# Kernel tuning notes

Measured on AMD Instinct MI355X. Metric: run time of the kernel, lower is better.

The kernel has to match this reference:

```python
import jax, jax.numpy as jnp
import numpy as np

B, T, DIM, H = 2, 2048, 512, 8
EPS = 1e-6


def setup_inputs() -> dict:
    key = jax.random.key(0)
    ks = jax.random.split(key, 6)
    scale = 0.05  # keep activations in a sane range for softmax/elu
    return {
        "x": jax.random.normal(ks[0], (B, T, DIM), dtype=jnp.float32),
        "Wq": jax.random.normal(ks[1], (DIM, DIM), dtype=jnp.float32) * scale,
        "Wk": jax.random.normal(ks[2], (DIM, DIM), dtype=jnp.float32) * scale,
        "Wv": jax.random.normal(ks[3], (DIM, DIM), dtype=jnp.float32) * scale,
        "Wo": jax.random.normal(ks[4], (DIM, DIM), dtype=jnp.float32) * scale,
        "bo": jax.random.normal(ks[5], (DIM,), dtype=jnp.float32) * scale,
    }


def reference(x, Wq, Wk, Wv, Wo, bo):
    b, t, dim = x.shape
    h = H
    d = dim // h
    # projections (nn.Linear: x @ W.T)
    q = x @ Wq.T
    k = x @ Wk.T
    v = x @ Wv.T
    mh = lambda z: z.reshape(b, t, h, d).transpose(0, 2, 1, 3)  # [b,h,t,d]
    q, k, v = mh(q), mh(k), mh(v)
    # causal linear attention with buckets = n (bucket size 1, no shift)
    q = jax.nn.softmax(q, axis=-1)
    k = jax.nn.elu(k) + 1.0  # psi
    k_cumsum = jnp.cumsum(k, axis=2)                       # [b,h,t,d]
    context = jnp.einsum('bhnd,bhne->bhnde', k, v)         # per-position outer products
    context = jnp.cumsum(context, axis=2)                  # causal prefix sum, [b,h,t,d,d]
    context = context / (k_cumsum[..., None] + EPS)        # safe_div
    attn = jnp.einsum('bhnd,bhnde->bhne', q, context)      # [b,h,t,d]
    out = attn.transpose(0, 2, 1, 3).reshape(b, t, dim)
    return out @ Wo.T + bo
```

## Files before the change

### kernel.cpp

```cpp
#include <hip/hip_runtime.h>

#define T_SEQ 2048
#define DIMM 512
#define NH 8
#define HD 64
#define BB 2
#define CHUNK 64
#define NCHUNK 32
#define EPSV 1e-6f
#define LDST 72

typedef __attribute__((ext_vector_type(8))) short bf16x8;
typedef __attribute__((ext_vector_type(4))) short s16x4;
typedef __attribute__((ext_vector_type(4))) float f32x4;

static __device__ inline short f2bf(float f) {
    union { float f; unsigned u; } v; v.f = f;
    unsigned r = v.u + 0x7FFFu + ((v.u >> 16) & 1u);
    return (short)(r >> 16);
}
static __device__ inline float bf2f(short s) {
    union { unsigned u; float f; } v; v.u = ((unsigned)(unsigned short)s) << 16;
    return v.f;
}

__global__ __launch_bounds__(256) void proj_mfma_kernel(
    const float* __restrict__ x, const float* __restrict__ Wq,
    const float* __restrict__ Wk, const float* __restrict__ Wv,
    short* __restrict__ Qs, short* __restrict__ Kbf,
    short* __restrict__ Ktb, short* __restrict__ Vt)
{
    __shared__ short As[128 * LDST];
    __shared__ short Bs[128 * LDST];
    const int which = blockIdx.y >> 2;
    const float* __restrict__ W = (which == 0) ? Wq : ((which == 1) ? Wk : Wv);
    const int m0 = blockIdx.x * 128;
    const int n0 = (blockIdx.y & 3) * 128;
    const int tid = threadIdx.x;
    const int lane = tid & 63, wid = tid >> 6;
    const int wr = wid >> 1, wc = wid & 1;
    const int fr = lane & 15, fg = lane >> 4;
    const int head0 = (blockIdx.y & 3) * 2 + wc;
    f32x4 acc[4][4] = {};
    for (int k0 = 0; k0 < DIMM; k0 += 64) {
        #pragma unroll
        for (int it = 0; it < 8; it++) {
            const int qi = it * 256 + tid;
            const int r = qi >> 4, k4 = (qi & 15) << 2;
            const float4 va = *(const float4*)(x + (size_t)(m0 + r) * DIMM + k0 + k4);
            *(s16x4*)&As[r * LDST + k4] = (s16x4){f2bf(va.x), f2bf(va.y), f2bf(va.z), f2bf(va.w)};
            const float4 vb = *(const float4*)(W + (size_t)(n0 + r) * DIMM + k0 + k4);
            *(s16x4*)&Bs[r * LDST + k4] = (s16x4){f2bf(vb.x), f2bf(vb.y), f2bf(vb.z), f2bf(vb.w)};
        }
        __syncthreads();
        #pragma unroll
        for (int ks = 0; ks < 2; ks++) {
            bf16x8 af[4], bfr[4];
            #pragma unroll
            for (int i = 0; i < 4; i++)
                af[i] = *(const bf16x8*)&As[(wr * 64 + i * 16 + fr) * LDST + ks * 32 + fg * 8];
            #pragma unroll
            for (int j = 0; j < 4; j++)
                bfr[j] = *(const bf16x8*)&Bs[(wc * 64 + j * 16 + fr) * LDST + ks * 32 + fg * 8];
            #pragma unroll
            for (int i = 0; i < 4; i++)
                #pragma unroll
                for (int j = 0; j < 4; j++)
                    acc[i][j] = __builtin_amdgcn_mfma_f32_16x16x32_bf16(af[i], bfr[j], acc[i][j], 0, 0, 0);
        }
        __syncthreads();
    }
    if (which == 0) {
        #pragma unroll
        for (int i = 0; i < 4; i++) {
            #pragma unroll
            for (int reg = 0; reg < 4; reg++) {
                float v[4];
                #pragma unroll
                for (int j = 0; j < 4; j++) v[j] = acc[i][j][reg];
                float mx = fmaxf(fmaxf(v[0], v[1]), fmaxf(v[2], v[3]));
                #pragma unroll
                for (int off = 1; off <= 8; off <<= 1) mx = fmaxf(mx, __shfl_xor(mx, off, 64));
                float e[4], s = 0.f;
                #pragma unroll
                for (int j = 0; j < 4; j++) { e[j] = __expf(v[j] - mx); s += e[j]; }
                #pragma unroll
                for (int off = 1; off <= 8; off <<= 1) s += __shfl_xor(s, off, 64);
                const float inv = 1.f / s;
                const int m = m0 + wr * 64 + i * 16 + fg * 4 + reg;
                const int b = m >> 11, t = m & (T_SEQ - 1);
                short* qp = Qs + (((size_t)(b * NH + head0)) * T_SEQ + t) * HD;
                #pragma unroll
                for (int j = 0; j < 4; j++) qp[j * 16 + fr] = f2bf(e[j] * inv);
            }
        }
    } else if (which == 1) {
        #pragma unroll
        for (int i = 0; i < 4; i++) {
            const int m3 = m0 + wr * 64 + i * 16 + fg * 4;
            const int b = m3 >> 11, t0 = m3 & (T_SEQ - 1);
            #pragma unroll
            for (int j = 0; j < 4; j++) {
                const int d = j * 16 + fr;
                short kv[4];
                #pragma unroll
                for (int reg = 0; reg < 4; reg++) {
                    float val = acc[i][j][reg];
                    val = (val > 0.f) ? (val + 1.f) : __expf(val);
                    kv[reg] = f2bf(val);
                }
                short* kp = Kbf + (((size_t)(b * NH + head0)) * T_SEQ + t0) * HD + d;
                kp[0] = kv[0]; kp[HD] = kv[1]; kp[2 * HD] = kv[2]; kp[3 * HD] = kv[3];
                *(s16x4*)(Ktb + (((size_t)(b * NH + head0)) * HD + d) * T_SEQ + t0) =
                    (s16x4){kv[0], kv[1], kv[2], kv[3]};
            }
        }
    } else {
        #pragma unroll
        for (int i = 0; i < 4; i++) {
            const int m3 = m0 + wr * 64 + i * 16 + fg * 4;
            const int b = m3 >> 11, t0 = m3 & (T_SEQ - 1);
            #pragma unroll
            for (int j = 0; j < 4; j++) {
                const int e = j * 16 + fr;
                *(s16x4*)(Vt + (((size_t)(b * NH + head0)) * HD + e) * T_SEQ + t0) =
                    (s16x4){f2bf(acc[i][j][0]), f2bf(acc[i][j][1]),
                            f2bf(acc[i][j][2]), f2bf(acc[i][j][3])};
            }
        }
    }
}

__global__ __launch_bounds__(256) void chunk_sum_kernel(
    const short* __restrict__ Ktb, const short* __restrict__ Vt,
    float* __restrict__ Schunk, float* __restrict__ kchunk)
{
    __shared__ short VtL[64 * LDST];
    __shared__ short KtL[64 * LDST];
    __shared__ float ksp[4][64];
    const int bh = blockIdx.x >> 5, c = blockIdx.x & 31;
    const int tid = threadIdx.x;
    const int lane = tid & 63, w = tid >> 6;
    const int fr = lane & 15, fg = lane >> 4;
    #pragma unroll
    for (int it = 0; it < 2; it++) {
        const int qi = it * 256 + tid;
        const int r = qi >> 3, c8 = (qi & 7) * 8;
        *(bf16x8*)&VtL[r * LDST + c8] =
            *(const bf16x8*)(Vt + ((size_t)(bh * HD) + r) * T_SEQ + c * CHUNK + c8);
        *(bf16x8*)&KtL[r * LDST + c8] =
            *(const bf16x8*)(Ktb + ((size_t)(bh * HD) + r) * T_SEQ + c * CHUNK + c8);
    }
    __syncthreads();
    f32x4 acc[4] = {};
    #pragma unroll
    for (int ks = 0; ks < 2; ks++) {
        const bf16x8 av = *(const bf16x8*)&VtL[(w * 16 + fr) * LDST + ks * 32 + fg * 8];
        #pragma unroll
        for (int j = 0; j < 4; j++) {
            const bf16x8 bk = *(const bf16x8*)&KtL[(j * 16 + fr) * LDST + ks * 32 + fg * 8];
            acc[j] = __builtin_amdgcn_mfma_f32_16x16x32_bf16(av, bk, acc[j], 0, 0, 0);
        }
    }
    float* Sout = Schunk + ((size_t)bh * NCHUNK + c) * 4096;
    #pragma unroll
    for (int j = 0; j < 4; j++)
        #pragma unroll
        for (int reg = 0; reg < 4; reg++)
            Sout[(w * 16 + fg * 4 + reg) * 64 + j * 16 + fr] = acc[j][reg];
    float ps = 0.f;
    #pragma unroll
    for (int t = 0; t < 16; t++) ps += bf2f(KtL[lane * LDST + w * 16 + t]);
    ksp[w][lane] = ps;
    __syncthreads();
    if (tid < 64)
        kchunk[((size_t)bh * NCHUNK + c) * 64 + tid] =
            ksp[0][tid] + ksp[1][tid] + ksp[2][tid] + ksp[3][tid];
}

__global__ __launch_bounds__(256) void scan_kernel(float* __restrict__ Schunk,
                                                   float* __restrict__ kchunk)
{
    const int gid = blockIdx.x * 256 + threadIdx.x;
    if (blockIdx.x < 256) {
        const int bh = gid >> 12, i = gid & 4095;
        float run = 0.f;
        float* p = Schunk + (size_t)bh * NCHUNK * 4096 + i;
        for (int c = 0; c < NCHUNK; c++) { const float tv = p[c * 4096]; p[c * 4096] = run; run += tv; }
    } else {
        const int idx = gid - 65536;
        const int bh = idx >> 6, d = idx & 63;
        float run = 0.f;
        float* p = kchunk + (size_t)bh * NCHUNK * 64 + d;
        for (int c = 0; c < NCHUNK; c++) { const float tv = p[c * 64]; p[c * 64] = run; run += tv; }
    }
}

__global__ __launch_bounds__(256) void intra_kernel(
    const short* __restrict__ Qs, const short* __restrict__ Kbf,
    const short* __restrict__ Vt, const float* __restrict__ Schunk,
    const float* __restrict__ kchunk, short* __restrict__ attnb)
{
    __shared__ short B1[64 * LDST];
    __shared__ short B2[64 * LDST];
    __shared__ short KL[64 * LDST];
    __shared__ short VtL[64 * LDST];
    __shared__ short QnL[64 * LDST];
    __shared__ float gsum[4][64];
    __shared__ float kpre[64];
    const int bh = blockIdx.x >> 5, c = blockIdx.x & 31;
    const int tid = threadIdx.x;
    const int lane = tid & 63, w = tid >> 6;
    const int fr = lane & 15, fg = lane >> 4;
    const size_t tdbase = ((size_t)bh * T_SEQ + c * CHUNK) * HD;
    #pragma unroll
    for (int it = 0; it < 2; it++) {
        const int qi = it * 256 + tid;
        const int r = qi >> 3, c8 = (qi & 7) * 8;
        *(bf16x8*)&B1[r * LDST + c8]  = *(const bf16x8*)(Qs + tdbase + r * HD + c8);
        *(bf16x8*)&KL[r * LDST + c8]  = *(const bf16x8*)(Kbf + tdbase + r * HD + c8);
        *(bf16x8*)&VtL[r * LDST + c8] =
            *(const bf16x8*)(Vt + ((size_t)(bh * HD) + r) * T_SEQ + c * CHUNK + c8);
    }
    {
        const float* Sp = Schunk + ((size_t)bh * NCHUNK + c) * 4096;
        #pragma unroll
        for (int it = 0; it < 4; it++) {
            const int qi = it * 256 + tid;
            const int r = qi >> 4, c4 = (qi & 15) * 4;
            const float4 v = *(const float4*)(Sp + r * 64 + c4);
            *(s16x4*)&B2[r * LDST + c4] = (s16x4){f2bf(v.x), f2bf(v.y), f2bf(v.z), f2bf(v.w)};
        }
    }
    if (tid < 64) kpre[tid] = kchunk[((size_t)bh * NCHUNK + c) * 64 + tid];
    __syncthreads();
    {
        float s = 0.f;
        #pragma unroll
        for (int t = 0; t < 16; t++) s += bf2f(KL[(w * 16 + t) * LDST + lane]);
        gsum[w][lane] = s;
    }
    __syncthreads();
    {
        float run = kpre[lane];
        for (int gg = 0; gg < w; gg++) run += gsum[gg][lane];
        #pragma unroll
        for (int t0 = 0; t0 < 16; t0++) {
            const int t = w * 16 + t0;
            run += bf2f(KL[t * LDST + lane]);
            const float qv = bf2f(B1[t * LDST + lane]);
            QnL[t * LDST + lane] = f2bf(qv / (run + EPSV));
        }
    }
    __syncthreads();
    {
        f32x4 a1[4] = {};
        #pragma unroll
        for (int ks = 0; ks < 2; ks++) {
            const bf16x8 aq = *(const bf16x8*)&QnL[(w * 16 + fr) * LDST + ks * 32 + fg * 8];
            #pragma unroll
            for (int j = 0; j < 4; j++) {
                const bf16x8 bk = *(const bf16x8*)&KL[(j * 16 + fr) * LDST + ks * 32 + fg * 8];
                a1[j] = __builtin_amdgcn_mfma_f32_16x16x32_bf16(aq, bk, a1[j], 0, 0, 0);
            }
        }
        const int trow = w * 16 + fg * 4;
        #pragma unroll
        for (int j = 0; j < 4; j++)
            #pragma unroll
            for (int reg = 0; reg < 4; reg++) {
                const int t = trow + reg, s = j * 16 + fr;
                B1[t * LDST + s] = (s <= t) ? f2bf(a1[j][reg]) : (short)0;
            }
    }
    __syncthreads();
    {
        f32x4 a2[4] = {};
        #pragma unroll
        for (int ks = 0; ks < 2; ks++) {
            const bf16x8 aq = *(const bf16x8*)&QnL[(w * 16 + fr) * LDST + ks * 32 + fg * 8];
            const bf16x8 aa = *(const bf16x8*)&B1[(w * 16 + fr) * LDST + ks * 32 + fg * 8];
            #pragma unroll
            for (int j = 0; j < 4; j++) {
                const bf16x8 bs = *(const bf16x8*)&B2[(j * 16 + fr) * LDST + ks * 32 + fg * 8];
                const bf16x8 bv = *(const bf16x8*)&VtL[(j * 16 + fr) * LDST + ks * 32 + fg * 8];
                a2[j] = __builtin_amdgcn_mfma_f32_16x16x32_bf16(aq, bs, a2[j], 0, 0, 0);
                a2[j] = __builtin_amdgcn_mfma_f32_16x16x32_bf16(aa, bv, a2[j], 0, 0, 0);
            }
        }
        short* ap = attnb + tdbase;
        const int trow = w * 16 + fg * 4;
        #pragma unroll
        for (int j = 0; j < 4; j++)
            #pragma unroll
            for (int reg = 0; reg < 4; reg++)
                ap[(trow + reg) * HD + j * 16 + fr] = f2bf(a2[j][reg]);
    }
}

__global__ __launch_bounds__(256) void outproj_mfma_kernel(
    const short* __restrict__ attnb, const float* __restrict__ Wo,
    const float* __restrict__ bo, float* __restrict__ out)
{
    __shared__ short As[128 * LDST];
    __shared__ short Bs[128 * LDST];
    const int m0 = blockIdx.x * 128;
    const int n0 = blockIdx.y * 128;
    const int tid = threadIdx.x;
    const int lane = tid & 63, wid = tid >> 6;
    const int wr = wid >> 1, wc = wid & 1;
    const int fr = lane & 15, fg = lane >> 4;
    f32x4 acc[4][4] = {};
    for (int k0 = 0; k0 < DIMM; k0 += 64) {
        const int h = k0 >> 6;
        #pragma unroll
        for (int it = 0; it < 4; it++) {
            const int qi = it * 256 + tid;
            const int r = qi >> 3, c8 = (qi & 7) * 8;
            const int m = m0 + r, b = m >> 11, t = m & (T_SEQ - 1);
            *(bf16x8*)&As[r * LDST + c8] =
                *(const bf16x8*)(attnb + (((size_t)(b * NH + h)) * T_SEQ + t) * HD + c8);
        }
        #pragma unroll
        for (int it = 0; it < 8; it++) {
            const int qi = it * 256 + tid;
            const int r = qi >> 4, k4 = (qi & 15) << 2;
            const float4 vb = *(const float4*)(Wo + (size_t)(n0 + r) * DIMM + k0 + k4);
            *(s16x4*)&Bs[r * LDST + k4] = (s16x4){f2bf(vb.x), f2bf(vb.y), f2bf(vb.z), f2bf(vb.w)};
        }
        __syncthreads();
        #pragma unroll
        for (int ks = 0; ks < 2; ks++) {
            bf16x8 af[4], bfr[4];
            #pragma unroll
            for (int i = 0; i < 4; i++)
                af[i] = *(const bf16x8*)&As[(wr * 64 + i * 16 + fr) * LDST + ks * 32 + fg * 8];
            #pragma unroll
            for (int j = 0; j < 4; j++)
                bfr[j] = *(const bf16x8*)&Bs[(wc * 64 + j * 16 + fr) * LDST + ks * 32 + fg * 8];
            #pragma unroll
            for (int i = 0; i < 4; i++)
                #pragma unroll
                for (int j = 0; j < 4; j++)
                    acc[i][j] = __builtin_amdgcn_mfma_f32_16x16x32_bf16(af[i], bfr[j], acc[i][j], 0, 0, 0);
        }
        __syncthreads();
    }
    #pragma unroll
    for (int i = 0; i < 4; i++) {
        #pragma unroll
        for (int j = 0; j < 4; j++) {
            #pragma unroll
            for (int reg = 0; reg < 4; reg++) {
                const int m = m0 + wr * 64 + i * 16 + fg * 4 + reg;
                const int n = n0 + wc * 64 + j * 16 + fr;
                out[(size_t)m * DIMM + n] = acc[i][j][reg] + bo[n];
            }
        }
    }
}

extern "C" void kernel_launch(void* const* d_in, const int* in_sizes, int n_in,
                              void* d_out, int out_size, void* d_ws, size_t ws_size,
                              hipStream_t stream)
{
    const float* x  = (const float*)d_in[0];
    const float* Wq = (const float*)d_in[1];
    const float* Wk = (const float*)d_in[2];
    const float* Wv = (const float*)d_in[3];
    const float* Wo = (const float*)d_in[4];
    const float* bo = (const float*)d_in[5];
    float* out = (float*)d_out;

    const size_t NELEM = (size_t)BB * T_SEQ * DIMM;
    short* Qs    = (short*)d_ws;
    short* Kbf   = Qs + NELEM;
    short* Ktb   = Kbf + NELEM;
    short* Vt    = Ktb + NELEM;
    short* attnb = Vt + NELEM;
    float* Schunk = (float*)(attnb + NELEM);
    float* kchunk = Schunk + (size_t)BB * NH * NCHUNK * 4096;

    proj_mfma_kernel<<<dim3(32, 12), 256, 0, stream>>>(x, Wq, Wk, Wv, Qs, Kbf, Ktb, Vt);
    chunk_sum_kernel<<<dim3(BB * NH * NCHUNK), 256, 0, stream>>>(Ktb, Vt, Schunk, kchunk);
    scan_kernel<<<dim3(260), 256, 0, stream>>>(Schunk, kchunk);
    intra_kernel<<<dim3(BB * NH * NCHUNK), 256, 0, stream>>>(Qs, Kbf, Vt, Schunk, kchunk, attnb);
    outproj_mfma_kernel<<<dim3(32, 4), 256, 0, stream>>>(attnb, Wo, bo, out);
}
```

Baseline: 60.74 us.

## Pre-convert inputs to bf16 and stage GEMM tiles via direct global-to-LDS loads

Adds a conversion kernel that writes x and all four weight matrices to bf16 once, concatenating Wq/Wk/Wv. The projection and output-projection GEMMs then load bf16 tiles straight into LDS with global_load_lds, with no register staging or in-loop conversion. This halves GEMM global read bytes and removes VALU conversion work. In exchange it adds an extra launch and pass over x, and drops the LDS row padding, which may cause bank conflicts on fragment reads.

```diff
diff --git a/kernel.cpp b/kernel.cpp
--- a/kernel.cpp
+++ b/kernel.cpp
@@ -23,34 +23,59 @@
     union { unsigned u; float f; } v; v.u = ((unsigned)(unsigned short)s) << 16;
     return v.f;
 }
-
-__global__ __launch_bounds__(256) void proj_mfma_kernel(
+static __device__ __forceinline__ void gload_lds16(const void* g, void* l) {
+    __builtin_amdgcn_global_load_lds(
+        (__attribute__((address_space(1))) void*)g,
+        (__attribute__((address_space(3))) void*)l, 16, 0, 0);
+}
+
+__global__ __launch_bounds__(256) void convert_kernel(
     const float* __restrict__ x, const float* __restrict__ Wq,
     const float* __restrict__ Wk, const float* __restrict__ Wv,
+    const float* __restrict__ Wo,
+    short* __restrict__ xb, short* __restrict__ Wcat, short* __restrict__ Wob)
+{
+    const int u = blockIdx.x * 256 + threadIdx.x;
+    const float* src; short* dst;
+    if (u < 262144) {
+        src = x + (size_t)u * 8; dst = xb + (size_t)u * 8;
+    } else {
+        const int v = u - 262144;
+        const int o = (v & 32767) * 8;
+        if (v < 32768)       { src = Wq + o; dst = Wcat + o; }
+        else if (v < 65536)  { src = Wk + o; dst = Wcat + 262144 + o; }
+        else if (v < 98304)  { src = Wv + o; dst = Wcat + 524288 + o; }
+        else                 { src = Wo + o; dst = Wob + o; }
+    }
+    const float4 a = *(const float4*)src;
+    const float4 b = *(const float4*)(src + 4);
+    *(bf16x8*)dst = (bf16x8){f2bf(a.x), f2bf(a.y), f2bf(a.z), f2bf(a.w),
+                             f2bf(b.x), f2bf(b.y), f2bf(b.z), f2bf(b.w)};
+}
+
+__global__ __launch_bounds__(256) void proj_mfma_kernel(
+    const short* __restrict__ xb, const short* __restrict__ Wcat,
     short* __restrict__ Qs, short* __restrict__ Kbf,
     short* __restrict__ Ktb, short* __restrict__ Vt)
 {
-    __shared__ short As[128 * LDST];
-    __shared__ short Bs[128 * LDST];
+    __shared__ short As[128 * 64];
+    __shared__ short Bs[128 * 64];
+    const int m0 = blockIdx.x * 128;
+    const int n0 = blockIdx.y * 128;
     const int which = blockIdx.y >> 2;
-    const float* __restrict__ W = (which == 0) ? Wq : ((which == 1) ? Wk : Wv);
-    const int m0 = blockIdx.x * 128;
-    const int n0 = (blockIdx.y & 3) * 128;
     const int tid = threadIdx.x;
-    const int lane = tid & 63, wid = tid >> 6;
-    const int wr = wid >> 1, wc = wid & 1;
+    const int lane = tid & 63, w = tid >> 6;
+    const int wr = w >> 1, wc = w & 1;
     const int fr = lane & 15, fg = lane >> 4;
+    const int lr = lane >> 3, lc = (lane & 7) * 8;
     const int head0 = (blockIdx.y & 3) * 2 + wc;
     f32x4 acc[4][4] = {};
     for (int k0 = 0; k0 < DIMM; k0 += 64) {
         #pragma unroll
-        for (int it = 0; it < 8; it++) {
-            const int qi = it * 256 + tid;
-            const int r = qi >> 4, k4 = (qi & 15) << 2;
-            const float4 va = *(const float4*)(x + (size_t)(m0 + r) * DIMM + k0 + k4);
-            *(s16x4*)&As[r * LDST + k4] = (s16x4){f2bf(va.x), f2bf(va.y), f2bf(va.z), f2bf(va.w)};
-            const float4 vb = *(const float4*)(W + (size_t)(n0 + r) * DIMM + k0 + k4);
-            *(s16x4*)&Bs[r * LDST + k4] = (s16x4){f2bf(vb.x), f2bf(vb.y), f2bf(vb.z), f2bf(vb.w)};
+        for (int it = 0; it < 4; it++) {
+            const int r0 = w * 32 + it * 8;
+            gload_lds16(xb + (size_t)(m0 + r0 + lr) * DIMM + k0 + lc, &As[r0 * 64]);
+            gload_lds16(Wcat + (size_t)(n0 + r0 + lr) * DIMM + k0 + lc, &Bs[r0 * 64]);
         }
         __syncthreads();
         #pragma unroll
@@ -58,10 +83,10 @@
             bf16x8 af[4], bfr[4];
             #pragma unroll
             for (int i = 0; i < 4; i++)
-                af[i] = *(const bf16x8*)&As[(wr * 64 + i * 16 + fr) * LDST + ks * 32 + fg * 8];
+                af[i] = *(const bf16x8*)&As[(wr * 64 + i * 16 + fr) * 64 + ks * 32 + fg * 8];
             #pragma unroll
             for (int j = 0; j < 4; j++)
-                bfr[j] = *(const bf16x8*)&Bs[(wc * 64 + j * 16 + fr) * LDST + ks * 32 + fg * 8];
+                bfr[j] = *(const bf16x8*)&Bs[(wc * 64 + j * 16 + fr) * 64 + ks * 32 + fg * 8];
             #pragma unroll
             for (int i = 0; i < 4; i++)
                 #pragma unroll
@@ -299,34 +324,28 @@
 }
 
 __global__ __launch_bounds__(256) void outproj_mfma_kernel(
-    const short* __restrict__ attnb, const float* __restrict__ Wo,
+    const short* __restrict__ attnb, const short* __restrict__ Wob,
     const float* __restrict__ bo, float* __restrict__ out)
 {
-    __shared__ short As[128 * LDST];
-    __shared__ short Bs[128 * LDST];
+    __shared__ short As[128 * 64];
+    __shared__ short Bs[128 * 64];
     const int m0 = blockIdx.x * 128;
     const int n0 = blockIdx.y * 128;
     const int tid = threadIdx.x;
-    const int lane = tid & 63, wid = tid >> 6;
-    const int wr = wid >> 1, wc = wid & 1;
+    const int lane = tid & 63, w = tid >> 6;
+    const int wr = w >> 1, wc = w & 1;
     const int fr = lane & 15, fg = lane >> 4;
+    const int lr = lane >> 3, lc = (lane & 7) * 8;
     f32x4 acc[4][4] = {};
     for (int k0 = 0; k0 < DIMM; k0 += 64) {
         const int h = k0 >> 6;
         #pragma unroll
         for (int it = 0; it < 4; it++) {
-            const int qi = it * 256 + tid;
-            const int r = qi >> 3, c8 = (qi & 7) * 8;
-            const int m = m0 + r, b = m >> 11, t = m & (T_SEQ - 1);
-            *(bf16x8*)&As[r * LDST + c8] =
-                *(const bf16x8*)(attnb + (((size_t)(b * NH + h)) * T_SEQ + t) * HD + c8);
-        }
-        #pragma unroll
-        for (int it = 0; it < 8; it++) {
-            const int qi = it * 256 + tid;
-            const int r = qi >> 4, k4 = (qi & 15) << 2;
-            const float4 vb = *(const float4*)(Wo + (size_t)(n0 + r) * DIMM + k0 + k4);
-            *(s16x4*)&Bs[r * LDST + k4] = (s16x4){f2bf(vb.x), f2bf(vb.y), f2bf(vb.z), f2bf(vb.w)};
+            const int r0 = w * 32 + it * 8;
+            const int m = m0 + r0 + lr;
+            const int b = m >> 11, t = m & (T_SEQ - 1);
+            gload_lds16(attnb + (((size_t)(b * NH + h)) * T_SEQ + t) * HD + lc, &As[r0 * 64]);
+            gload_lds16(Wob + (size_t)(n0 + r0 + lr) * DIMM + k0 + lc, &Bs[r0 * 64]);
         }
         __syncthreads();
         #pragma unroll
@@ -334,10 +353,10 @@
             bf16x8 af[4], bfr[4];
             #pragma unroll
             for (int i = 0; i < 4; i++)
-                af[i] = *(const bf16x8*)&As[(wr * 64 + i * 16 + fr) * LDST + ks * 32 + fg * 8];
+                af[i] = *(const bf16x8*)&As[(wr * 64 + i * 16 + fr) * 64 + ks * 32 + fg * 8];
             #pragma unroll
             for (int j = 0; j < 4; j++)
-                bfr[j] = *(const bf16x8*)&Bs[(wc * 64 + j * 16 + fr) * LDST + ks * 32 + fg * 8];
+                bfr[j] = *(const bf16x8*)&Bs[(wc * 64 + j * 16 + fr) * 64 + ks * 32 + fg * 8];
             #pragma unroll
             for (int i = 0; i < 4; i++)
                 #pragma unroll
@@ -373,7 +392,10 @@
     float* out = (float*)d_out;
 
     const size_t NELEM = (size_t)BB * T_SEQ * DIMM;
-    short* Qs    = (short*)d_ws;
+    short* xb    = (short*)d_ws;
+    short* Wcat  = xb + NELEM;
+    short* Wob   = Wcat + 786432;
+    short* Qs    = Wob + 262144;
     short* Kbf   = Qs + NELEM;
     short* Ktb   = Kbf + NELEM;
     short* Vt    = Ktb + NELEM;
@@ -381,9 +403,10 @@
     float* Schunk = (float*)(attnb + NELEM);
     float* kchunk = Schunk + (size_t)BB * NH * NCHUNK * 4096;
 
-    proj_mfma_kernel<<<dim3(32, 12), 256, 0, stream>>>(x, Wq, Wk, Wv, Qs, Kbf, Ktb, Vt);
+    convert_kernel<<<dim3(1536), 256, 0, stream>>>(x, Wq, Wk, Wv, Wo, xb, Wcat, Wob);
+    proj_mfma_kernel<<<dim3(32, 12), 256, 0, stream>>>(xb, Wcat, Qs, Kbf, Ktb, Vt);
     chunk_sum_kernel<<<dim3(BB * NH * NCHUNK), 256, 0, stream>>>(Ktb, Vt, Schunk, kchunk);
     scan_kernel<<<dim3(260), 256, 0, stream>>>(Schunk, kchunk);
     intra_kernel<<<dim3(BB * NH * NCHUNK), 256, 0, stream>>>(Qs, Kbf, Vt, Schunk, kchunk, attnb);
-    outproj_mfma_kernel<<<dim3(32, 4), 256, 0, stream>>>(attnb, Wo, bo, out);
-}
+    outproj_mfma_kernel<<<dim3(32, 4), 256, 0, stream>>>(attnb, Wob, bo, out);
+}
```

New measurement: 61.62 us. Within noise of the previous version (+1.5%).
